# Performance work log

Measured on AMD Instinct MI355X. Metric: run time of the kernel, lower is better.

The kernel has to match this reference:

```python
import jax, jax.numpy as jnp
import numpy as np

N_PATTERNS = 16384
D_FEAT = 1024
BATCH = 512
MAX_ITER = 8
BETA = 1.0


def sparsemax_axis0(z):
    """Sparsemax (Euclidean projection onto the simplex) along axis 0. z: [N, B]."""
    n = z.shape[0]
    zs = -jnp.sort(-z, axis=0)                       # descending sort, [N, B]
    k = jnp.arange(1, n + 1, dtype=z.dtype)[:, None]  # [N, 1]
    cssv = jnp.cumsum(zs, axis=0) - 1.0              # cumulative sum minus 1
    cond = zs - cssv / k > 0                         # support condition
    ksup = jnp.sum(cond, axis=0)                     # [B] support size per column
    tau = jnp.take_along_axis(cssv / k, (ksup - 1)[None, :], axis=0)  # [1, B]
    return jnp.maximum(z - tau, 0.0)


def setup_inputs() -> dict:
    key = jax.random.key(0)
    kx, kq = jax.random.split(key)
    X = jax.random.normal(kx, (N_PATTERNS, D_FEAT), dtype=jnp.float32)
    Q = jax.random.normal(kq, (D_FEAT, BATCH), dtype=jnp.float32)
    return {"X": X, "Q": Q, "return_p": 1}


def reference(X, Q, return_p):
    # ypsi='none' -> identity applied to X and Q before the loop (no-op).
    # yomega='entmax' with alpha=2.0 -> sparsemax(beta * X @ Q, dim=0).
    p = None
    for _ in range(MAX_ITER):
        p = sparsemax_axis0(BETA * (X @ Q))  # [N, B]
        Q = X.T @ p                           # [d, B]; ypsi identity
    if return_p:
        return p
    return Q
```

## Files before the change

kernel.cpp:

```cpp
#include <hip/hip_runtime.h>
#include <hip/hip_bf16.h>

#define NPAT  16384
#define DF    1024
#define BATCH 512
#define CAP   256
#define SUP   16
#define MAXIT 8

typedef __attribute__((ext_vector_type(8))) short short8v;
typedef __attribute__((ext_vector_type(4))) float f32x4;
typedef unsigned short ushortT;

#define GLD16(gp, lp) __builtin_amdgcn_global_load_lds( \
    (const __attribute__((address_space(1))) void*)(gp), \
    (__attribute__((address_space(3))) void*)(lp), 16, 0, 0)

__device__ __forceinline__ unsigned encf(float f) {
  unsigned u = __float_as_uint(f);
  return (u & 0x80000000u) ? ~u : (u | 0x80000000u);
}
__device__ __forceinline__ float decf(unsigned e) {
  unsigned u = (e & 0x80000000u) ? (e & 0x7FFFFFFFu) : ~e;
  return __uint_as_float(u);
}

__device__ __forceinline__ void bsplit(float x, ushortT& h, ushortT& l) {
  __hip_bfloat16 hb = __float2bfloat16(x);
  float hf = __bfloat162float(hb);
  __hip_bfloat16 lb = __float2bfloat16(x - hf);
  h = *(ushortT*)&hb;
  l = *(ushortT*)&lb;
}

__global__ void k_xsplit(const float4* __restrict__ X4, unsigned* __restrict__ Xh,
                         unsigned* __restrict__ Xl) {
  size_t i = (size_t)blockIdx.x * blockDim.x + threadIdx.x;
  float4 v = X4[i];
  ushortT h0, h1, h2, h3, l0, l1, l2, l3;
  bsplit(v.x, h0, l0); bsplit(v.y, h1, l1);
  bsplit(v.z, h2, l2); bsplit(v.w, h3, l3);
  Xh[2 * i]     = (unsigned)h0 | ((unsigned)h1 << 16);
  Xh[2 * i + 1] = (unsigned)h2 | ((unsigned)h3 << 16);
  Xl[2 * i]     = (unsigned)l0 | ((unsigned)l1 << 16);
  Xl[2 * i + 1] = (unsigned)l2 | ((unsigned)l3 << 16);
}

__global__ void k_qprep(const float* __restrict__ Q, unsigned* __restrict__ Qh,
                        unsigned* __restrict__ Ql, unsigned* __restrict__ colMaxEnc,
                        int* __restrict__ candCount) {
  __shared__ float tile[32][33];
  int tx = threadIdx.x & 31;
  int ty = threadIdx.x >> 5;
  int n0 = blockIdx.x * 32;
  int k0 = blockIdx.y * 32;
  if (blockIdx.y == 0 && blockIdx.x < 2) {
    colMaxEnc[blockIdx.x * 256 + threadIdx.x] = 0u;
    candCount[blockIdx.x * 256 + threadIdx.x] = 0;
  }
#pragma unroll
  for (int s = 0; s < 4; ++s)
    tile[ty + 8 * s][tx] = Q[(size_t)(k0 + ty + 8 * s) * BATCH + n0 + tx];
  __syncthreads();
  int r = threadIdx.x >> 4;
  int p = threadIdx.x & 15;
#pragma unroll
  for (int s = 0; s < 2; ++s) {
    int rr = r + 16 * s;
    float a = tile[2 * p][rr], b = tile[2 * p + 1][rr];
    ushortT ha, la, hb, lb;
    bsplit(a, ha, la); bsplit(b, hb, lb);
    size_t o = ((size_t)(n0 + rr) * DF + k0) / 2 + p;
    Qh[o] = (unsigned)ha | ((unsigned)hb << 16);
    Ql[o] = (unsigned)la | ((unsigned)lb << 16);
  }
}

__global__ __launch_bounds__(256, 2) void k_gemm(
    const ushortT* __restrict__ Xh, const ushortT* __restrict__ Xl,
    const ushortT* __restrict__ Qh, const ushortT* __restrict__ Ql,
    unsigned* __restrict__ colMaxEnc, int* __restrict__ candCount,
    int* __restrict__ candIdx, float* __restrict__ candVal,
    const int* __restrict__ conv) {
  if (*conv) return;
  __shared__ ushortT Ah[128 * 64], Al[128 * 64], Bh[128 * 64], Bl[128 * 64];
  __shared__ unsigned cmax[128];
  __shared__ float cthr[128];
  const int t  = threadIdx.x;
  const int l  = t & 63;
  const int w  = t >> 6;
  const int wr = w >> 1, wc = w & 1;
  const int lr = l & 15;
  const int lk = l >> 4;
  const int lin = blockIdx.y * 4 + blockIdx.x;
  const int nid = (lin & 7) * 64 + (lin >> 3);
  const int bx = nid & 3, by = nid >> 2;
  const int row0 = by * 128, col0 = bx * 128;

  f32x4 acc[4][4];
#pragma unroll
  for (int i = 0; i < 4; ++i)
#pragma unroll
    for (int j = 0; j < 4; ++j) acc[i][j] = (f32x4)0.f;

  int rA[4], sA[4], dstB[4];
#pragma unroll
  for (int i = 0; i < 4; ++i) {
    int id = i * 256 + t;
    int r = id >> 3, c = id & 7;
    rA[i]   = r;
    sA[i]   = ((c ^ (r & 7)) << 3);
    dstB[i] = (i * 256 + (t & 192)) * 8;
  }

  for (int kc = 0; kc < 16; ++kc) {
    int kb = kc * 64;
    __syncthreads();
#pragma unroll
    for (int i = 0; i < 4; ++i) {
      size_t ao = (size_t)(row0 + rA[i]) * DF + kb + sA[i];
      size_t bo = (size_t)(col0 + rA[i]) * DF + kb + sA[i];
      GLD16(Xh + ao, &Ah[dstB[i]]);
      GLD16(Xl + ao, &Al[dstB[i]]);
      GLD16(Qh + bo, &Bh[dstB[i]]);
      GLD16(Ql + bo, &Bl[dstB[i]]);
    }
    __syncthreads();
#pragma unroll
    for (int pass = 0; pass < 3; ++pass) {
      const ushortT* As = (pass == 2) ? Al : Ah;
      const ushortT* Bs = (pass == 1) ? Bl : Bh;
#pragma unroll
      for (int kk = 0; kk < 2; ++kk) {
        short8v af[4], bf[4];
#pragma unroll
        for (int i = 0; i < 4; ++i) {
          int row = wr * 64 + i * 16 + lr;
          int ch = (kk * 4 + lk) ^ (row & 7);
          af[i] = *(const short8v*)(&As[row * 64 + ch * 8]);
        }
#pragma unroll
        for (int j = 0; j < 4; ++j) {
          int col = wc * 64 + j * 16 + lr;
          int ch = (kk * 4 + lk) ^ (col & 7);
          bf[j] = *(const short8v*)(&Bs[col * 64 + ch * 8]);
        }
#pragma unroll
        for (int i = 0; i < 4; ++i)
#pragma unroll
          for (int j = 0; j < 4; ++j)
            acc[i][j] = __builtin_amdgcn_mfma_f32_16x16x32_bf16(af[i], bf[j], acc[i][j], 0, 0, 0);
      }
    }
  }

  __syncthreads();
  if (t < 128) cmax[t] = 0u;
  __syncthreads();
#pragma unroll
  for (int j = 0; j < 4; ++j) {
    float cm = -3.4e38f;
#pragma unroll
    for (int i = 0; i < 4; ++i)
#pragma unroll
      for (int q = 0; q < 4; ++q) cm = fmaxf(cm, acc[i][j][q]);
    cm = fmaxf(cm, __shfl_xor(cm, 16));
    cm = fmaxf(cm, __shfl_xor(cm, 32));
    if (lk == 0) atomicMax(&cmax[wc * 64 + j * 16 + lr], encf(cm));
  }
  __syncthreads();
  if (t < 128) {
    unsigned old = atomicMax(&colMaxEnc[col0 + t], cmax[t]);
    unsigned snap = old > cmax[t] ? old : cmax[t];
    cthr[t] = decf(snap) - 1.0f;
  }
  __syncthreads();
#pragma unroll
  for (int j = 0; j < 4; ++j) {
    int cl = wc * 64 + j * 16 + lr;
    float thr = cthr[cl];
    int gcol = col0 + cl;
#pragma unroll
    for (int i = 0; i < 4; ++i) {
      int rbase = row0 + wr * 64 + i * 16 + lk * 4;
#pragma unroll
      for (int q = 0; q < 4; ++q) {
        float v = acc[i][j][q];
        if (v > thr) {
          int p = atomicAdd(&candCount[gcol], 1);
          if (p < CAP) {
            candIdx[p * BATCH + gcol] = rbase + q;
            candVal[p * BATCH + gcol] = v;
          }
        }
      }
    }
  }
}

__global__ __launch_bounds__(256) void k_post(
    int* __restrict__ candCount, const int* __restrict__ candIdx,
    const float* __restrict__ candVal, unsigned* __restrict__ colMaxEnc,
    int* __restrict__ prevK, int* __restrict__ prevIdx, float* __restrict__ prevP,
    const float* __restrict__ X, unsigned* __restrict__ Qh, unsigned* __restrict__ Ql,
    int* __restrict__ conv, int* __restrict__ sameCount, int* __restrict__ doneCount,
    float* __restrict__ out, int doQupd) {
  if (*conv) return;
  const int b = blockIdx.x;
  const int t = threadIdx.x;
  __shared__ float scv[SUP];
  __shared__ int   sci[SUP];
  __shared__ float scw[SUP];
  __shared__ int scnt, sk;

  int m = candCount[b];
  if (m > CAP) m = CAP;
  float thr = decf(colMaxEnc[b]) - 1.0f;
  if (t == 0) scnt = 0;
  __syncthreads();
  if (t < m) {
    float v = candVal[t * BATCH + b];
    if (v > thr) {
      int p = atomicAdd(&scnt, 1);
      if (p < SUP) { scv[p] = v; sci[p] = candIdx[t * BATCH + b]; }
    }
  }
  __syncthreads();

  if (t == 0) {
    int n = scnt < SUP ? scnt : SUP;
    float cv[SUP]; int ci[SUP];
    for (int j = 0; j < n; ++j) { cv[j] = scv[j]; ci[j] = sci[j]; }
    for (int j = 1; j < n; ++j) {
      float v = cv[j]; int id = ci[j];
      int s = j - 1;
      while (s >= 0 && (cv[s] < v || (cv[s] == v && ci[s] > id))) {
        cv[s + 1] = cv[s]; ci[s + 1] = ci[s]; --s;
      }
      cv[s + 1] = v; ci[s + 1] = id;
    }
    float cum = 0.f; int k = 0; float tau = 0.f;
    for (int j = 0; j < n; ++j) {
      cum += cv[j];
      float tj = (cum - 1.0f) / (float)(j + 1);
      if (cv[j] > tj) { k = j + 1; tau = tj; }
    }
    int pk = prevK[b];
    for (int j = 0; j < pk && j < SUP; ++j)
      out[(size_t)prevIdx[b * SUP + j] * BATCH + b] = 0.f;
    int same = (k == pk);
    for (int j = 0; j < k; ++j) {
      float p = cv[j] - tau;
      same = same && (ci[j] == prevIdx[b * SUP + j]) && (p == prevP[b * SUP + j]);
      prevIdx[b * SUP + j] = ci[j];
      prevP[b * SUP + j]   = p;
      out[(size_t)ci[j] * BATCH + b] = p;
      scw[j] = p; sci[j] = ci[j];
    }
    prevK[b] = k;
    sk = k;
    colMaxEnc[b] = 0u;
    candCount[b] = 0;
    if (same) atomicAdd(sameCount, 1);
    __threadfence();
    int d = atomicAdd(doneCount, 1);
    if (d == BATCH - 1) {
      __threadfence();
      if (atomicAdd(sameCount, 0) == BATCH) atomicExch(conv, 1);
      atomicExch(sameCount, 0);
      atomicExch(doneCount, 0);
    }
  }
  __syncthreads();

  if (doQupd) {
    int k = sk;
    float a0 = 0.f, a1 = 0.f, a2 = 0.f, a3 = 0.f;
    for (int j = 0; j < k; ++j) {
      float wgt = scw[j];
      const float* xr = X + (size_t)sci[j] * DF;
      a0 += wgt * xr[2 * t];
      a1 += wgt * xr[2 * t + 1];
      a2 += wgt * xr[512 + 2 * t];
      a3 += wgt * xr[512 + 2 * t + 1];
    }
    ushortT h0, h1, h2, h3, l0, l1, l2, l3;
    bsplit(a0, h0, l0); bsplit(a1, h1, l1);
    bsplit(a2, h2, l2); bsplit(a3, h3, l3);
    Qh[b * 512 + t]       = (unsigned)h0 | ((unsigned)h1 << 16);
    Ql[b * 512 + t]       = (unsigned)l0 | ((unsigned)l1 << 16);
    Qh[b * 512 + 256 + t] = (unsigned)h2 | ((unsigned)h3 << 16);
    Ql[b * 512 + 256 + t] = (unsigned)l2 | ((unsigned)l3 << 16);
  }
}

extern "C" void kernel_launch(void* const* d_in, const int* in_sizes, int n_in,
                              void* d_out, int out_size, void* d_ws, size_t ws_size,
                              hipStream_t stream) {
  const float* X = (const float*)d_in[0];
  const float* Q = (const float*)d_in[1];
  float* out = (float*)d_out;

  char* ws = (char*)d_ws;
  ushortT*  Xh  = (ushortT*)ws;             ws += (size_t)NPAT * DF * 2;
  ushortT*  Xl  = (ushortT*)ws;             ws += (size_t)NPAT * DF * 2;
  ushortT*  Qh  = (ushortT*)ws;             ws += (size_t)BATCH * DF * 2;
  ushortT*  Ql  = (ushortT*)ws;             ws += (size_t)BATCH * DF * 2;
  unsigned* colMaxEnc = (unsigned*)ws;      ws += BATCH * 4;
  int*      candCount = (int*)ws;           ws += BATCH * 4;
  int*      candIdx   = (int*)ws;           ws += BATCH * CAP * 4;
  float*    candVal   = (float*)ws;         ws += BATCH * CAP * 4;
  int*      prevK     = (int*)ws;           ws += BATCH * 4;
  int*      prevIdx   = (int*)ws;           ws += BATCH * SUP * 4;
  float*    prevP     = (float*)ws;         ws += BATCH * SUP * 4;
  int*      conv      = (int*)ws;           ws += 4;
  int*      sameCount = (int*)ws;           ws += 4;
  int*      doneCount = (int*)ws;

  (void)hipMemsetAsync(d_out, 0, (size_t)out_size * sizeof(float), stream);
  (void)hipMemsetAsync(conv, 0, 12, stream);

  k_xsplit<<<NPAT * DF / 4 / 256, 256, 0, stream>>>((const float4*)X, (unsigned*)Xh, (unsigned*)Xl);
  k_qprep<<<dim3(BATCH / 32, DF / 32), 256, 0, stream>>>(Q, (unsigned*)Qh, (unsigned*)Ql,
                                                         colMaxEnc, candCount);

  for (int it = 0; it < MAXIT; ++it) {
    k_gemm<<<dim3(4, 128), 256, 0, stream>>>(Xh, Xl, Qh, Ql, colMaxEnc, candCount,
                                             candIdx, candVal, conv);
    k_post<<<BATCH, 256, 0, stream>>>(candCount, candIdx, candVal, colMaxEnc,
                                      prevK, prevIdx, prevP,
                                      X, (unsigned*)Qh, (unsigned*)Ql,
                                      conv, sameCount, doneCount,
                                      out, it < MAXIT - 1 ? 1 : 0);
  }
}
```

Before: 333.0 us.

## Track per-column convergence with active lists and skip converged columns

New measurement: 307.6 us. 1.08x faster.

```diff
diff --git a/kernel.cpp b/kernel.cpp
--- a/kernel.cpp
+++ b/kernel.cpp
@@ -48,15 +48,19 @@
 
 __global__ void k_qprep(const float* __restrict__ Q, unsigned* __restrict__ Qh,
                         unsigned* __restrict__ Ql, unsigned* __restrict__ colMaxEnc,
-                        int* __restrict__ candCount) {
+                        int* __restrict__ candCount, int* __restrict__ listA,
+                        int* __restrict__ cntA, int* __restrict__ cntB) {
   __shared__ float tile[32][33];
   int tx = threadIdx.x & 31;
   int ty = threadIdx.x >> 5;
   int n0 = blockIdx.x * 32;
   int k0 = blockIdx.y * 32;
   if (blockIdx.y == 0 && blockIdx.x < 2) {
-    colMaxEnc[blockIdx.x * 256 + threadIdx.x] = 0u;
-    candCount[blockIdx.x * 256 + threadIdx.x] = 0;
+    int idx = blockIdx.x * 256 + threadIdx.x;
+    colMaxEnc[idx] = 0u;
+    candCount[idx] = 0;
+    listA[idx] = idx;
+    if (idx == 0) { *cntA = BATCH; *cntB = 0; }
   }
 #pragma unroll
   for (int s = 0; s < 4; ++s)
@@ -81,8 +85,8 @@
     const ushortT* __restrict__ Qh, const ushortT* __restrict__ Ql,
     unsigned* __restrict__ colMaxEnc, int* __restrict__ candCount,
     int* __restrict__ candIdx, float* __restrict__ candVal,
-    const int* __restrict__ conv) {
-  if (*conv) return;
+    const int* __restrict__ actList, const int* __restrict__ cntIn,
+    int* __restrict__ cntOut) {
   __shared__ ushortT Ah[128 * 64], Al[128 * 64], Bh[128 * 64], Bl[128 * 64];
   __shared__ unsigned cmax[128];
   __shared__ float cthr[128];
@@ -95,7 +99,11 @@
   const int lin = blockIdx.y * 4 + blockIdx.x;
   const int nid = (lin & 7) * 64 + (lin >> 3);
   const int bx = nid & 3, by = nid >> 2;
-  const int row0 = by * 128, col0 = bx * 128;
+  const int row0 = by * 128;
+
+  if (bx == 0 && by == 0 && t == 0) *cntOut = 0;
+  const int nAct = *cntIn;
+  if (bx * 128 >= nAct) return;
 
   f32x4 acc[4][4];
 #pragma unroll
@@ -104,6 +112,7 @@
     for (int j = 0; j < 4; ++j) acc[i][j] = (f32x4)0.f;
 
   int rA[4], sA[4], dstB[4];
+  size_t colB[4];
 #pragma unroll
   for (int i = 0; i < 4; ++i) {
     int id = i * 256 + t;
@@ -111,6 +120,8 @@
     rA[i]   = r;
     sA[i]   = ((c ^ (r & 7)) << 3);
     dstB[i] = (i * 256 + (t & 192)) * 8;
+    int cc = bx * 128 + r;
+    colB[i] = (size_t)actList[cc < nAct ? cc : 0] * DF;
   }
 
   for (int kc = 0; kc < 16; ++kc) {
@@ -119,7 +130,7 @@
 #pragma unroll
     for (int i = 0; i < 4; ++i) {
       size_t ao = (size_t)(row0 + rA[i]) * DF + kb + sA[i];
-      size_t bo = (size_t)(col0 + rA[i]) * DF + kb + sA[i];
+      size_t bo = colB[i] + kb + sA[i];
       GLD16(Xh + ao, &Ah[dstB[i]]);
       GLD16(Xl + ao, &Al[dstB[i]]);
       GLD16(Qh + bo, &Bh[dstB[i]]);
@@ -170,16 +181,22 @@
   }
   __syncthreads();
   if (t < 128) {
-    unsigned old = atomicMax(&colMaxEnc[col0 + t], cmax[t]);
-    unsigned snap = old > cmax[t] ? old : cmax[t];
-    cthr[t] = decf(snap) - 1.0f;
+    int cc = bx * 128 + t;
+    if (cc < nAct) {
+      int gcol = actList[cc];
+      unsigned old = atomicMax(&colMaxEnc[gcol], cmax[t]);
+      unsigned snap = old > cmax[t] ? old : cmax[t];
+      cthr[t] = decf(snap) - 1.0f;
+    } else {
+      cthr[t] = 3.4e38f;
+    }
   }
   __syncthreads();
 #pragma unroll
   for (int j = 0; j < 4; ++j) {
     int cl = wc * 64 + j * 16 + lr;
     float thr = cthr[cl];
-    int gcol = col0 + cl;
+    int gcol = actList[bx * 128 + cl];
 #pragma unroll
     for (int i = 0; i < 4; ++i) {
       int rbase = row0 + wr * 64 + i * 16 + lk * 4;
@@ -203,10 +220,12 @@
     const float* __restrict__ candVal, unsigned* __restrict__ colMaxEnc,
     int* __restrict__ prevK, int* __restrict__ prevIdx, float* __restrict__ prevP,
     const float* __restrict__ X, unsigned* __restrict__ Qh, unsigned* __restrict__ Ql,
-    int* __restrict__ conv, int* __restrict__ sameCount, int* __restrict__ doneCount,
+    const int* __restrict__ actList, const int* __restrict__ cntIn,
+    int* __restrict__ listOut, int* __restrict__ cntOut,
     float* __restrict__ out, int doQupd) {
-  if (*conv) return;
-  const int b = blockIdx.x;
+  const int nAct = *cntIn;
+  if ((int)blockIdx.x >= nAct) return;
+  const int b = actList[blockIdx.x];
   const int t = threadIdx.x;
   __shared__ float scv[SUP];
   __shared__ int   sci[SUP];
@@ -261,14 +280,9 @@
     sk = k;
     colMaxEnc[b] = 0u;
     candCount[b] = 0;
-    if (same) atomicAdd(sameCount, 1);
-    __threadfence();
-    int d = atomicAdd(doneCount, 1);
-    if (d == BATCH - 1) {
-      __threadfence();
-      if (atomicAdd(sameCount, 0) == BATCH) atomicExch(conv, 1);
-      atomicExch(sameCount, 0);
-      atomicExch(doneCount, 0);
+    if (!same) {
+      int pos = atomicAdd(cntOut, 1);
+      listOut[pos] = b;
     }
   }
   __syncthreads();
@@ -313,24 +327,30 @@
   int*      prevK     = (int*)ws;           ws += BATCH * 4;
   int*      prevIdx   = (int*)ws;           ws += BATCH * SUP * 4;
   float*    prevP     = (float*)ws;         ws += BATCH * SUP * 4;
-  int*      conv      = (int*)ws;           ws += 4;
-  int*      sameCount = (int*)ws;           ws += 4;
-  int*      doneCount = (int*)ws;
+  int*      listA     = (int*)ws;           ws += BATCH * 4;
+  int*      listB     = (int*)ws;           ws += BATCH * 4;
+  int*      cntA      = (int*)ws;           ws += 4;
+  int*      cntB      = (int*)ws;
 
   (void)hipMemsetAsync(d_out, 0, (size_t)out_size * sizeof(float), stream);
-  (void)hipMemsetAsync(conv, 0, 12, stream);
 
   k_xsplit<<<NPAT * DF / 4 / 256, 256, 0, stream>>>((const float4*)X, (unsigned*)Xh, (unsigned*)Xl);
   k_qprep<<<dim3(BATCH / 32, DF / 32), 256, 0, stream>>>(Q, (unsigned*)Qh, (unsigned*)Ql,
-                                                         colMaxEnc, candCount);
+                                                         colMaxEnc, candCount,
+                                                         listA, cntA, cntB);
 
   for (int it = 0; it < MAXIT; ++it) {
+    int*  inList  = (it & 1) ? listB : listA;
+    int*  inCnt   = (it & 1) ? cntB  : cntA;
+    int*  outList = (it & 1) ? listA : listB;
+    int*  outCnt  = (it & 1) ? cntA  : cntB;
     k_gemm<<<dim3(4, 128), 256, 0, stream>>>(Xh, Xl, Qh, Ql, colMaxEnc, candCount,
-                                             candIdx, candVal, conv);
+                                             candIdx, candVal,
+                                             inList, inCnt, outCnt);
     k_post<<<BATCH, 256, 0, stream>>>(candCount, candIdx, candVal, colMaxEnc,
                                       prevK, prevIdx, prevP,
                                       X, (unsigned*)Qh, (unsigned*)Ql,
-                                      conv, sameCount, doneCount,
+                                      inList, inCnt, outList, outCnt,
                                       out, it < MAXIT - 1 ? 1 : 0);
   }
 }
```
